# Performance work log

Hardware: AMD Instinct MI355X
Metric: run time of the kernel (lower is better)

The kernel has to match this reference:

```python
import jax, jax.numpy as jnp
import numpy as np

N = 4096
BATCH = 1024


def setup_inputs() -> dict:
    key = jax.random.key(0)
    k1, k2, k3 = jax.random.split(key, 3)
    stdv = 1.0 / np.sqrt(N)
    return {
        "input": jax.random.normal(k1, (BATCH, N), dtype=jnp.float32),
        "weight": jax.random.uniform(k2, (N,), dtype=jnp.float32, minval=-stdv, maxval=stdv),
        "bias": jax.random.uniform(k3, (N,), dtype=jnp.float32, minval=-stdv, maxval=stdv),
    }


def reference(input, weight, bias):
    # Krylov(shift, w) has columns K[:, k] = shift^k(w), i.e. K[i, k] = w[(i - k) mod n].
    # F.linear(x, K.T, b) = x @ (K.T).T + b = x @ K + b.
    n = weight.shape[0]
    i = jnp.arange(n)
    idx = (i[:, None] - i[None, :]) % n        # [n, n] circulant index pattern
    K = weight[idx]                            # [n, n] circulant matrix
    return input @ K + bias
```

## Files before the change

### kernel.cpp

```cpp
#include <hip/hip_runtime.h>

typedef short s8v __attribute__((ext_vector_type(8)));
typedef float f4v __attribute__((ext_vector_type(4)));
typedef float f16v __attribute__((ext_vector_type(16)));

#define ND 4096
#define NMASK 4095

__device__ __forceinline__ unsigned short f2bf(float f) {
  __bf16 h = (__bf16)f;
  return __builtin_bit_cast(unsigned short, h);
}

__device__ __forceinline__ void gload_lds16(const void* g, void* l) {
  __builtin_amdgcn_global_load_lds(
      (const __attribute__((address_space(1))) unsigned int*)g,
      (__attribute__((address_space(3))) unsigned int*)l, 16, 0, 0);
}

__global__ __launch_bounds__(256)
void prep(const float* __restrict__ X, const float* __restrict__ W,
          unsigned short* __restrict__ Xpk, unsigned int* __restrict__ wlg) {
  const int b = blockIdx.x;
  const int tid = threadIdx.x;
  if (b < 1024) {
    const int r0 = (b & 15) << 6;
    const int k0 = (b >> 4) << 6;
    const int r = tid >> 2;
    const int kseg = tid & 3;
    const int row = r0 + r;
    const int k = k0 + (kseg << 4);
    const float* src = X + row * ND + k;
    const f4v g0 = *(const f4v*)(src + 0);
    const f4v g1 = *(const f4v*)(src + 4);
    const f4v g2 = *(const f4v*)(src + 8);
    const f4v g3 = *(const f4v*)(src + 12);
    s8v u0, u1;
    #pragma unroll
    for (int j = 0; j < 4; ++j) {
      u0[j] = (short)f2bf(g0[j]); u0[4 + j] = (short)f2bf(g1[j]);
      u1[j] = (short)f2bf(g2[j]); u1[4 + j] = (short)f2bf(g3[j]);
    }
    const int o0 = k >> 3;
    *(s8v*)(Xpk + ((o0 * 1024 + row) << 3))       = u0;
    *(s8v*)(Xpk + (((o0 + 1) * 1024 + row) << 3)) = u1;
  } else {
    const int m = (b - 1024) * 256 + tid;
    const int e0 = m << 1, e1 = e0 + 1;
    const int i0 = ((e0 >> 3) + (e0 & 7)) & NMASK;
    const int i1 = ((e1 >> 3) + (e1 & 7)) & NMASK;
    wlg[m] = (unsigned int)f2bf(W[i0]) | ((unsigned int)f2bf(W[i1]) << 16);
  }
}

__global__ __launch_bounds__(512, 4)
void circ_mm(const unsigned short* __restrict__ Xpk,
             const unsigned short* __restrict__ wlg,
             const float* __restrict__ bias, float* __restrict__ C) {
  extern __shared__ unsigned short smem[];
  unsigned char* __restrict__ sb = (unsigned char*)smem;

  const int tid = threadIdx.x;
  const int bid = blockIdx.x;
  const int x = bid & 7;
  const int i = bid >> 3;
  const int m0 = (x + ((i >> 5) << 3)) << 6;
  const int n0 = (i & 31) << 7;

  const int lane = tid & 63;
  const int wv = tid >> 6;
  const int wv1024 = wv << 10;

  #pragma unroll
  for (int it = 0; it < 8; ++it) {
    const int b = it * 8192 + wv1024;
    gload_lds16((const unsigned char*)wlg + b + lane * 16, sb + b);
  }

  const int lc = lane & 31;
  const int lh = lane >> 5;
  const int lh8 = lh << 3;
  const int wn = wv & 1;
  const int kb = wv >> 1;

  const unsigned short* gXa =
      Xpk + ((((kb << 1) + lh) << 10) + m0 + lc) * 8;

  int s0 = ((kb << 4) + lh8 - (n0 + wn * 64 + 0 * 32 + lc)) & NMASK;
  int s1 = ((kb << 4) + lh8 - (n0 + wn * 64 + 1 * 32 + lc)) & NMASK;

  f16v acc[2][2];
  #pragma unroll
  for (int mf = 0; mf < 2; ++mf)
    #pragma unroll
    for (int nf = 0; nf < 2; ++nf)
      #pragma unroll
      for (int e = 0; e < 16; ++e) acc[mf][nf][e] = 0.f;

  s8v Ac0 = *(const s8v*)(gXa + 0);
  s8v Ac1 = *(const s8v*)(gXa + 256);
  __syncthreads();
  s8v Bc0 = *(const s8v*)(sb + (s0 << 4));
  s8v Bc1 = *(const s8v*)(sb + (s1 << 4));

  #pragma unroll 2
  for (int t = 0; t < 64; ++t) {
    s8v An0, An1, Bn0, Bn1;
    if (t < 63) {
      const unsigned short* gp = gXa + (t + 1) * 65536;
      An0 = *(const s8v*)(gp + 0);
      An1 = *(const s8v*)(gp + 256);
      s0 = (s0 + 64) & NMASK;
      s1 = (s1 + 64) & NMASK;
      Bn0 = *(const s8v*)(sb + (s0 << 4));
      Bn1 = *(const s8v*)(sb + (s1 << 4));
    }

    __builtin_amdgcn_s_setprio(1);
    acc[0][0] = __builtin_amdgcn_mfma_f32_32x32x16_bf16(Ac0, Bc0, acc[0][0], 0, 0, 0);
    acc[1][0] = __builtin_amdgcn_mfma_f32_32x32x16_bf16(Ac1, Bc0, acc[1][0], 0, 0, 0);
    acc[0][1] = __builtin_amdgcn_mfma_f32_32x32x16_bf16(Ac0, Bc1, acc[0][1], 0, 0, 0);
    acc[1][1] = __builtin_amdgcn_mfma_f32_32x32x16_bf16(Ac1, Bc1, acc[1][1], 0, 0, 0);
    __builtin_amdgcn_s_setprio(0);

    Ac0 = An0; Ac1 = An1; Bc0 = Bn0; Bc1 = Bn1;
  }

  __syncthreads();
  float* red = (float*)smem;
  float* rb;

  if (kb >= 2) {
    rb = red + ((kb - 2) * 2 + wn) * 4096;
    #pragma unroll
    for (int mf = 0; mf < 2; ++mf)
      #pragma unroll
      for (int nf = 0; nf < 2; ++nf)
        #pragma unroll
        for (int q = 0; q < 4; ++q) {
          const int j = ((mf * 2 + nf) * 4 + q);
          f4v v;
          #pragma unroll
          for (int e = 0; e < 4; ++e) v[e] = acc[mf][nf][q * 4 + e];
          *(f4v*)(&rb[(j * 64 + lane) * 4]) = v;
        }
  }
  __syncthreads();
  if (kb < 2) {
    rb = red + (kb * 2 + wn) * 4096;
    #pragma unroll
    for (int mf = 0; mf < 2; ++mf)
      #pragma unroll
      for (int nf = 0; nf < 2; ++nf)
        #pragma unroll
        for (int q = 0; q < 4; ++q) {
          const int j = ((mf * 2 + nf) * 4 + q);
          const f4v v = *(const f4v*)(&rb[(j * 64 + lane) * 4]);
          #pragma unroll
          for (int e = 0; e < 4; ++e) acc[mf][nf][q * 4 + e] += v[e];
        }
  }
  __syncthreads();
  if (kb == 1) {
    rb = red + wn * 4096;
    #pragma unroll
    for (int mf = 0; mf < 2; ++mf)
      #pragma unroll
      for (int nf = 0; nf < 2; ++nf)
        #pragma unroll
        for (int q = 0; q < 4; ++q) {
          const int j = ((mf * 2 + nf) * 4 + q);
          f4v v;
          #pragma unroll
          for (int e = 0; e < 4; ++e) v[e] = acc[mf][nf][q * 4 + e];
          *(f4v*)(&rb[(j * 64 + lane) * 4]) = v;
        }
  }
  __syncthreads();
  if (kb == 0) {
    rb = red + wn * 4096;
    #pragma unroll
    for (int mf = 0; mf < 2; ++mf)
      #pragma unroll
      for (int nf = 0; nf < 2; ++nf)
        #pragma unroll
        for (int q = 0; q < 4; ++q) {
          const int j = ((mf * 2 + nf) * 4 + q);
          const f4v v = *(const f4v*)(&rb[(j * 64 + lane) * 4]);
          #pragma unroll
          for (int e = 0; e < 4; ++e) acc[mf][nf][q * 4 + e] += v[e];
        }
    const int lh4 = lh << 2;
    #pragma unroll
    for (int nf = 0; nf < 2; ++nf) {
      const int col = n0 + wn * 64 + nf * 32 + lc;
      const float bv = bias[col];
      #pragma unroll
      for (int mf = 0; mf < 2; ++mf)
        #pragma unroll
        for (int g = 0; g < 4; ++g) {
          const int row = m0 + mf * 32 + g * 8 + lh4;
          #pragma unroll
          for (int e = 0; e < 4; ++e)
            C[(row + e) * ND + col] = acc[mf][nf][g * 4 + e] + bv;
        }
    }
  }
}

extern "C" void kernel_launch(void* const* d_in, const int* in_sizes, int n_in,
                              void* d_out, int out_size, void* d_ws, size_t ws_size,
                              hipStream_t stream) {
  (void)hipFuncSetAttribute((const void*)circ_mm,
                            hipFuncAttributeMaxDynamicSharedMemorySize, 65536);
  const float* X    = (const float*)d_in[0];
  const float* W    = (const float*)d_in[1];
  const float* bias = (const float*)d_in[2];
  unsigned short* wlg = (unsigned short*)d_ws;
  unsigned short* Xpk = (unsigned short*)d_ws + 32768;

  prep<<<dim3(1088), dim3(256), 0, stream>>>(X, W, Xpk, (unsigned int*)wlg);
  circ_mm<<<dim3(512), dim3(512), 65536, stream>>>(Xpk, wlg, bias, (float*)d_out);
}
```

Baseline: 43.43 us.

## Halve circ_mm block to 4 waves, each covering full 128-column tile

The circulant GEMM block drops from 8 waves to 4. Each wave now covers all 128 output columns (4 N-fragments) instead of 64, so every A fragment loaded from global memory feeds twice as many MFMAs and redundant A loads across the former wn pair go away. The cost is twice the accumulator registers per wave (occupancy bound lowered to 2 blocks/CU), fewer waves to hide latency, and a longer serial K-loop per wave.

Result: faster. 41.50 us (-4.4%).

```diff
diff --git a/kernel.cpp b/kernel.cpp
--- a/kernel.cpp
+++ b/kernel.cpp
@@ -53,7 +53,7 @@
   }
 }
 
-__global__ __launch_bounds__(512, 4)
+__global__ __launch_bounds__(256, 2)
 void circ_mm(const unsigned short* __restrict__ Xpk,
              const unsigned short* __restrict__ wlg,
              const float* __restrict__ bias, float* __restrict__ C) {
@@ -69,31 +69,31 @@
 
   const int lane = tid & 63;
   const int wv = tid >> 6;
-  const int wv1024 = wv << 10;
+  const int kb = wv;
 
   #pragma unroll
-  for (int it = 0; it < 8; ++it) {
-    const int b = it * 8192 + wv1024;
+  for (int it = 0; it < 16; ++it) {
+    const int b = it * 4096 + (wv << 10);
     gload_lds16((const unsigned char*)wlg + b + lane * 16, sb + b);
   }
 
   const int lc = lane & 31;
   const int lh = lane >> 5;
   const int lh8 = lh << 3;
-  const int wn = wv & 1;
-  const int kb = wv >> 1;
 
   const unsigned short* gXa =
       Xpk + ((((kb << 1) + lh) << 10) + m0 + lc) * 8;
 
-  int s0 = ((kb << 4) + lh8 - (n0 + wn * 64 + 0 * 32 + lc)) & NMASK;
-  int s1 = ((kb << 4) + lh8 - (n0 + wn * 64 + 1 * 32 + lc)) & NMASK;
-
-  f16v acc[2][2];
+  int s0 = ((kb << 4) + lh8 - (n0 + 0 * 32 + lc)) & NMASK;
+  int s1 = ((kb << 4) + lh8 - (n0 + 1 * 32 + lc)) & NMASK;
+  int s2 = ((kb << 4) + lh8 - (n0 + 2 * 32 + lc)) & NMASK;
+  int s3 = ((kb << 4) + lh8 - (n0 + 3 * 32 + lc)) & NMASK;
+
+  f16v acc[2][4];
   #pragma unroll
   for (int mf = 0; mf < 2; ++mf)
     #pragma unroll
-    for (int nf = 0; nf < 2; ++nf)
+    for (int nf = 0; nf < 4; ++nf)
       #pragma unroll
       for (int e = 0; e < 16; ++e) acc[mf][nf][e] = 0.f;
 
@@ -102,18 +102,24 @@
   __syncthreads();
   s8v Bc0 = *(const s8v*)(sb + (s0 << 4));
   s8v Bc1 = *(const s8v*)(sb + (s1 << 4));
+  s8v Bc2 = *(const s8v*)(sb + (s2 << 4));
+  s8v Bc3 = *(const s8v*)(sb + (s3 << 4));
 
   #pragma unroll 2
   for (int t = 0; t < 64; ++t) {
-    s8v An0, An1, Bn0, Bn1;
+    s8v An0, An1, Bn0, Bn1, Bn2, Bn3;
     if (t < 63) {
       const unsigned short* gp = gXa + (t + 1) * 65536;
       An0 = *(const s8v*)(gp + 0);
       An1 = *(const s8v*)(gp + 256);
       s0 = (s0 + 64) & NMASK;
       s1 = (s1 + 64) & NMASK;
+      s2 = (s2 + 64) & NMASK;
+      s3 = (s3 + 64) & NMASK;
       Bn0 = *(const s8v*)(sb + (s0 << 4));
       Bn1 = *(const s8v*)(sb + (s1 << 4));
+      Bn2 = *(const s8v*)(sb + (s2 << 4));
+      Bn3 = *(const s8v*)(sb + (s3 << 4));
     }
 
     __builtin_amdgcn_s_setprio(1);
@@ -121,9 +127,14 @@
     acc[1][0] = __builtin_amdgcn_mfma_f32_32x32x16_bf16(Ac1, Bc0, acc[1][0], 0, 0, 0);
     acc[0][1] = __builtin_amdgcn_mfma_f32_32x32x16_bf16(Ac0, Bc1, acc[0][1], 0, 0, 0);
     acc[1][1] = __builtin_amdgcn_mfma_f32_32x32x16_bf16(Ac1, Bc1, acc[1][1], 0, 0, 0);
+    acc[0][2] = __builtin_amdgcn_mfma_f32_32x32x16_bf16(Ac0, Bc2, acc[0][2], 0, 0, 0);
+    acc[1][2] = __builtin_amdgcn_mfma_f32_32x32x16_bf16(Ac1, Bc2, acc[1][2], 0, 0, 0);
+    acc[0][3] = __builtin_amdgcn_mfma_f32_32x32x16_bf16(Ac0, Bc3, acc[0][3], 0, 0, 0);
+    acc[1][3] = __builtin_amdgcn_mfma_f32_32x32x16_bf16(Ac1, Bc3, acc[1][3], 0, 0, 0);
     __builtin_amdgcn_s_setprio(0);
 
-    Ac0 = An0; Ac1 = An1; Bc0 = Bn0; Bc1 = Bn1;
+    Ac0 = An0; Ac1 = An1;
+    Bc0 = Bn0; Bc1 = Bn1; Bc2 = Bn2; Bc3 = Bn3;
   }
 
   __syncthreads();
@@ -131,14 +142,14 @@
   float* rb;
 
   if (kb >= 2) {
-    rb = red + ((kb - 2) * 2 + wn) * 4096;
-    #pragma unroll
-    for (int mf = 0; mf < 2; ++mf)
-      #pragma unroll
-      for (int nf = 0; nf < 2; ++nf)
-        #pragma unroll
-        for (int q = 0; q < 4; ++q) {
-          const int j = ((mf * 2 + nf) * 4 + q);
+    rb = red + (kb - 2) * 8192;
+    #pragma unroll
+    for (int mf = 0; mf < 2; ++mf)
+      #pragma unroll
+      for (int nf = 0; nf < 4; ++nf)
+        #pragma unroll
+        for (int q = 0; q < 4; ++q) {
+          const int j = (mf * 4 + nf) * 4 + q;
           f4v v;
           #pragma unroll
           for (int e = 0; e < 4; ++e) v[e] = acc[mf][nf][q * 4 + e];
@@ -147,14 +158,14 @@
   }
   __syncthreads();
   if (kb < 2) {
-    rb = red + (kb * 2 + wn) * 4096;
-    #pragma unroll
-    for (int mf = 0; mf < 2; ++mf)
-      #pragma unroll
-      for (int nf = 0; nf < 2; ++nf)
-        #pragma unroll
-        for (int q = 0; q < 4; ++q) {
-          const int j = ((mf * 2 + nf) * 4 + q);
+    rb = red + kb * 8192;
+    #pragma unroll
+    for (int mf = 0; mf < 2; ++mf)
+      #pragma unroll
+      for (int nf = 0; nf < 4; ++nf)
+        #pragma unroll
+        for (int q = 0; q < 4; ++q) {
+          const int j = (mf * 4 + nf) * 4 + q;
           const f4v v = *(const f4v*)(&rb[(j * 64 + lane) * 4]);
           #pragma unroll
           for (int e = 0; e < 4; ++e) acc[mf][nf][q * 4 + e] += v[e];
@@ -162,14 +173,14 @@
   }
   __syncthreads();
   if (kb == 1) {
-    rb = red + wn * 4096;
-    #pragma unroll
-    for (int mf = 0; mf < 2; ++mf)
-      #pragma unroll
-      for (int nf = 0; nf < 2; ++nf)
-        #pragma unroll
-        for (int q = 0; q < 4; ++q) {
-          const int j = ((mf * 2 + nf) * 4 + q);
+    rb = red;
+    #pragma unroll
+    for (int mf = 0; mf < 2; ++mf)
+      #pragma unroll
+      for (int nf = 0; nf < 4; ++nf)
+        #pragma unroll
+        for (int q = 0; q < 4; ++q) {
+          const int j = (mf * 4 + nf) * 4 + q;
           f4v v;
           #pragma unroll
           for (int e = 0; e < 4; ++e) v[e] = acc[mf][nf][q * 4 + e];
@@ -178,22 +189,22 @@
   }
   __syncthreads();
   if (kb == 0) {
-    rb = red + wn * 4096;
-    #pragma unroll
-    for (int mf = 0; mf < 2; ++mf)
-      #pragma unroll
-      for (int nf = 0; nf < 2; ++nf)
-        #pragma unroll
-        for (int q = 0; q < 4; ++q) {
-          const int j = ((mf * 2 + nf) * 4 + q);
+    rb = red;
+    #pragma unroll
+    for (int mf = 0; mf < 2; ++mf)
+      #pragma unroll
+      for (int nf = 0; nf < 4; ++nf)
+        #pragma unroll
+        for (int q = 0; q < 4; ++q) {
+          const int j = (mf * 4 + nf) * 4 + q;
           const f4v v = *(const f4v*)(&rb[(j * 64 + lane) * 4]);
           #pragma unroll
           for (int e = 0; e < 4; ++e) acc[mf][nf][q * 4 + e] += v[e];
         }
     const int lh4 = lh << 2;
     #pragma unroll
-    for (int nf = 0; nf < 2; ++nf) {
-      const int col = n0 + wn * 64 + nf * 32 + lc;
+    for (int nf = 0; nf < 4; ++nf) {
+      const int col = n0 + nf * 32 + lc;
       const float bv = bias[col];
       #pragma unroll
       for (int mf = 0; mf < 2; ++mf)
@@ -220,5 +231,5 @@
   unsigned short* Xpk = (unsigned short*)d_ws + 32768;
 
   prep<<<dim3(1088), dim3(256), 0, stream>>>(X, W, Xpk, (unsigned int*)wlg);
-  circ_mm<<<dim3(512), dim3(512), 65536, stream>>>(Xpk, wlg, bias, (float*)d_out);
-}
+  circ_mm<<<dim3(512), dim3(256), 65536, stream>>>(Xpk, wlg, bias, (float*)d_out);
+}
```
